# Performance work log

Measured on AMD Instinct MI355X. Metric: run time of the kernel, lower is better.

## Reference

```python
import jax, jax.numpy as jnp
import numpy as np

BEAM = 64  # beam_size from init (0 < 64 < num_tags=1024)


def setup_inputs() -> dict:
    key = jax.random.key(0)
    k1, k2, k3 = jax.random.split(key, 3)
    S, T = 16384, 1024  # seq_len, num_tags
    scores = jax.random.normal(k1, (S, T), dtype=jnp.float32)
    weights = jax.random.normal(k2, (T, T), dtype=jnp.float32) * 0.1  # CRF transition params
    tags = jax.random.randint(k3, (S,), 0, T)
    return {"scores": scores, "weights": weights, "tags": tags}


def reference(scores, weights, tags):
    # scores: [S, T] emission scores (output of base RNN tagger)
    # weights: [T, T] CRF transition scores, tags: [S] gold tags (eval mode, tags given)
    best_scores, best_tags = jax.lax.top_k(scores, BEAM)  # [S, B]

    def step(carry, x):
        vit, fwd = carry                     # each [B]
        prev_t, cur_t, cur_s = x             # [B], [B], [B]
        w = weights[prev_t[:, None], cur_t[None, :]]          # [B, B] transition lookup
        vals_v = vit[:, None] + cur_s[None, :] + w            # Viterbi lattice [B, B]
        vals_f = fwd[:, None] + cur_s[None, :] + w            # forward lattice [B, B]
        new_vit = vals_v.max(axis=0)
        bp = jnp.argmax(vals_v, axis=0)                       # backpointer [B]
        new_fwd = jax.nn.logsumexp(vals_f, axis=0)
        return (new_vit, new_fwd), bp

    init = (best_scores[0], best_scores[0])
    (vit, fwd), bps = jax.lax.scan(
        step, init, (best_tags[:-1], best_tags[1:], best_scores[1:]))  # bps: [S-1, B]

    # Viterbi backtrace
    last = jnp.argmax(vit)

    def back(idx, bp):
        new = bp[idx]
        return new, new

    _, idxs = jax.lax.scan(back, last, bps, reverse=True)     # indices for steps 0..S-2
    best_indices = jnp.concatenate([idxs, last[None]])        # [S]
    predicted_tags = jnp.take_along_axis(best_tags, best_indices[:, None], axis=1)[:, 0]

    # negative log-likelihood
    base = jnp.take_along_axis(scores, tags[:, None], axis=1).sum()
    crf = weights[tags[:-1], tags[1:]].sum()
    logZ = jax.nn.logsumexp(fwd)
    logprob = base + crf - logZ
    return predicted_tags, -logprob
```

## Files before the change

### kernel.cpp

```cpp
#include <hip/hip_runtime.h>
#include <math.h>

#define S 16384
#define T 1024
#define B 64
#define NSTEP (S - 1)
#define CH 64
#define NC 256
#define PD 8

#define K2E 1.44269504088896340736f
#define LN2 0.69314718055994530942f
#define LN64 4.15888308335967186f

static constexpr size_t SZ_SB   = (size_t)S * B * 4;
static constexpr size_t OFF_BS  = 0;
static constexpr size_t OFF_BT  = OFF_BS + SZ_SB;
static constexpr size_t OFF_VIT = OFF_BT + SZ_SB;
static constexpr size_t OFF_BP  = OFF_VIT + SZ_SB;
static constexpr size_t OFF_GT  = OFF_BP + SZ_SB;
static constexpr size_t SZ_GT   = (size_t)NC * B * B * 4;
static constexpr size_t OFF_MAP = OFF_GT + SZ_GT;
static constexpr size_t OFF_BND = OFF_MAP + (size_t)NC * B * 4;
static constexpr size_t OFF_SCAL= OFF_BND + 4096;
static constexpr size_t OFF_W   = OFF_SCAL + 4096;
static constexpr size_t SZ_W    = (size_t)NSTEP * B * B * 4;

__global__ __launch_bounds__(64) void k_topk(const float* __restrict__ scores,
                                             float* __restrict__ bs, int* __restrict__ bt) {
  int row = blockIdx.x;
  int lane = threadIdx.x;
  const float* rp = scores + (size_t)row * T;
  float v[16];
#pragma unroll
  for (int k = 0; k < 16; ++k) v[k] = rp[k * 64 + lane];
  for (int b = 0; b < B; ++b) {
    float lv = v[0]; int lk = 0;
#pragma unroll
    for (int k = 1; k < 16; ++k) {
      if (v[k] > lv) { lv = v[k]; lk = k; }
    }
    float bv = lv; int be = lk * 64 + lane;
#pragma unroll
    for (int off = 32; off >= 1; off >>= 1) {
      float ov = __shfl_xor(bv, off);
      int   oe = __shfl_xor(be, off);
      if (ov > bv || (ov == bv && oe < be)) { bv = ov; be = oe; }
    }
    if (lane == 0) {
      bs[(size_t)row * B + b] = bv;
      bt[(size_t)row * B + b] = be;
    }
    int bk = be >> 6, bl = be & 63;
#pragma unroll
    for (int k = 0; k < 16; ++k) {
      if (k == bk && lane == bl) v[k] = -3.0e38f;
    }
  }
}

__global__ __launch_bounds__(256) void k_pregather(const float* __restrict__ wt,
                                                   const int* __restrict__ bt,
                                                   float* __restrict__ Wp,
                                                   int tbase, int ns) {
  size_t n = (size_t)blockIdx.x * 256 + threadIdx.x;
  int i4  = (int)(n & 15);
  int j   = (int)((n >> 4) & 63);
  int rel = (int)(n >> 10);
  if (rel >= ns) return;
  int tm1 = tbase - 1 + rel;
  int ct = bt[(size_t)(tm1 + 1) * B + j];
  const int* pt = bt + (size_t)tm1 * B + i4 * 4;
  float4 o;
  o.x = wt[(size_t)pt[0] * T + ct];
  o.y = wt[(size_t)pt[1] * T + ct];
  o.z = wt[(size_t)pt[2] * T + ct];
  o.w = wt[(size_t)pt[3] * T + ct];
  ((float4*)Wp)[n] = o;
}

__global__ __launch_bounds__(512) void k_seqvit_seg(const float* __restrict__ bs,
                                                    const float* __restrict__ Wp,
                                                    float* __restrict__ vit,
                                                    int t0, int ns) {
  __shared__ alignas(16) float vb[2][B];
  int tid = threadIdx.x, w = tid >> 6, l = tid & 63;
  int j = (w << 3) | (l >> 3);
  int i0 = (l & 7) << 3;
  if (tid < B) {
    float v0 = (t0 == 1) ? bs[tid] : vit[(size_t)(t0 - 1) * B + tid];
    vb[0][tid] = v0;
    if (t0 == 1) vit[tid] = v0;
  }
  const float* wrow = Wp + (size_t)j * B + i0;
  float4 wa[PD], wc[PD];
  float ss[PD];
#pragma unroll
  for (int d = 0; d < PD; ++d) {
    if (d < ns) {
      const float4* q = (const float4*)(wrow + (size_t)d * B * B);
      wa[d] = q[0]; wc[d] = q[1];
      ss[d] = bs[(size_t)(t0 + d) * B + j];
    }
  }
  __syncthreads();
  int p = 0;
  for (int k0 = 0; k0 < ns; k0 += PD) {
#pragma unroll
    for (int ph = 0; ph < PD; ++ph) {
      int k = k0 + ph;
      if (k < ns) {
        float4 A = wa[ph], C = wc[ph];
        float s = ss[ph];
        const float4* vr = (const float4*)&vb[p][i0];
        float4 va = vr[0], v2 = vr[1];
        float m0 = fmaxf((va.x + s) + A.x, (va.y + s) + A.y);
        float m1 = fmaxf((va.z + s) + A.z, (va.w + s) + A.w);
        float m2 = fmaxf((v2.x + s) + C.x, (v2.y + s) + C.y);
        float m3 = fmaxf((v2.z + s) + C.z, (v2.w + s) + C.w);
        float m = fmaxf(fmaxf(m0, m1), fmaxf(m2, m3));
        m = fmaxf(m, __shfl_xor(m, 1));
        m = fmaxf(m, __shfl_xor(m, 2));
        m = fmaxf(m, __shfl_xor(m, 4));
        if (k + PD < ns) {
          const float4* q = (const float4*)(wrow + (size_t)(k + PD) * B * B);
          wa[ph] = q[0]; wc[ph] = q[1];
          ss[ph] = bs[(size_t)(t0 + k + PD) * B + j];
        }
        if ((l & 7) == 0) {
          vb[1 - p][j] = m;
          vit[(size_t)(t0 + k) * B + j] = m;
        }
        __syncthreads();
        p ^= 1;
      }
    }
  }
}

__global__ __launch_bounds__(512) void k_seqvit_slow(const float* __restrict__ bs,
                                                     const int* __restrict__ bt,
                                                     const float* __restrict__ wt,
                                                     float* __restrict__ vit) {
  __shared__ float vitbuf[B];
  __shared__ int tagbuf[B];
  __shared__ float part[2][8][B];
  int tid = threadIdx.x, w = tid >> 6, j = tid & 63;
  float v0 = bs[j];
  vitbuf[j] = v0;
  tagbuf[j] = bt[j];
  if (w == 0) vit[j] = v0;
  __syncthreads();
  for (int t = 1; t <= NSTEP; ++t) {
    float ss = bs[(size_t)t * B + j];
    int ct = bt[(size_t)t * B + j];
    float m = -3.0e38f;
#pragma unroll
    for (int e = 0; e < 8; ++e) {
      float vi = vitbuf[(w << 3) + e];
      int   pt = tagbuf[(w << 3) + e];
      float wv = wt[(size_t)pt * T + ct];
      m = fmaxf(m, (vi + ss) + wv);
    }
    int par = t & 1;
    part[par][w][j] = m;
    __syncthreads();
    float nv = part[par][0][j];
#pragma unroll
    for (int ww = 1; ww < 8; ++ww) nv = fmaxf(nv, part[par][ww][j]);
    vitbuf[j] = nv;
    tagbuf[j] = ct;
    if (w == 0) vit[(size_t)t * B + j] = nv;
  }
}

__global__ __launch_bounds__(256) void k_fwdchunk(const float* __restrict__ bs,
                                                  const int* __restrict__ bt,
                                                  const float* __restrict__ Wp,
                                                  const float* __restrict__ wt,
                                                  float* __restrict__ Gt, int usePre) {
  __shared__ alignas(16) float Pt[2][B][68];
  __shared__ float X[B][B];
  __shared__ alignas(16) float Rk[B];
  __shared__ float Qi[B];
  __shared__ float pmx[4][B];
  __shared__ int ptl[B];
  int tid = threadIdx.x, r = tid >> 6, j = tid & 63;
  int c = blockIdx.x;
  int t0 = c * CH + 1;
  int t1 = min(c * CH + CH, NSTEP);
#pragma unroll
  for (int e = 0; e < 16; ++e) {
    int i = 16 * r + e;
    Pt[0][j][i] = (i == j) ? 1.0f : 0.0f;
  }
  if (r == 0) { Rk[j] = 0.0f; Qi[j] = 0.0f; }
  __syncthreads();
  int pb = 0;
  for (int t = t0; t <= t1; ++t) {
    float ev[16];
    if (usePre) {
      const float4* q = (const float4*)(Wp + (((size_t)(t - 1) * B + j) * B + 16 * r));
      float4 q0 = q[0], q1 = q[1], q2 = q[2], q3 = q[3];
      ev[0] = q0.x; ev[1] = q0.y; ev[2] = q0.z; ev[3] = q0.w;
      ev[4] = q1.x; ev[5] = q1.y; ev[6] = q1.z; ev[7] = q1.w;
      ev[8] = q2.x; ev[9] = q2.y; ev[10] = q2.z; ev[11] = q2.w;
      ev[12] = q3.x; ev[13] = q3.y; ev[14] = q3.z; ev[15] = q3.w;
    } else {
      if (tid < B) ptl[tid] = bt[(size_t)(t - 1) * B + tid];
      __syncthreads();
      int ct = bt[(size_t)t * B + j];
#pragma unroll
      for (int e = 0; e < 16; ++e) ev[e] = wt[(size_t)ptl[16 * r + e] * T + ct];
    }
    {
      const float4* rq = (const float4*)&Rk[16 * r];
      float4 r0 = rq[0], r1 = rq[1], r2 = rq[2], r3 = rq[3];
      ev[0] += r0.x; ev[1] += r0.y; ev[2] += r0.z; ev[3] += r0.w;
      ev[4] += r1.x; ev[5] += r1.y; ev[6] += r1.z; ev[7] += r1.w;
      ev[8] += r2.x; ev[9] += r2.y; ev[10] += r2.z; ev[11] += r2.w;
      ev[12] += r3.x; ev[13] += r3.y; ev[14] += r3.z; ev[15] += r3.w;
    }
    float pm = ev[0];
#pragma unroll
    for (int e = 1; e < 16; ++e) pm = fmaxf(pm, ev[e]);
    pmx[r][j] = pm;
    __syncthreads();
    float Mw = fmaxf(fmaxf(pmx[0][j], pmx[1][j]), fmaxf(pmx[2][j], pmx[3][j]));
#pragma unroll
    for (int e = 0; e < 16; ++e)
      X[16 * r + e][j] = exp2f(K2E * (ev[e] - Mw) - 6.0f);
    __syncthreads();
    if (r == 0) Rk[j] = (bs[(size_t)t * B + j] + Mw) + LN64;
    float acc[16];
#pragma unroll
    for (int e = 0; e < 16; ++e) acc[e] = 0.0f;
    for (int k = 0; k < B; ++k) {
      float xk = X[k][j];
      const float4* pr = (const float4*)&Pt[pb][k][16 * r];
      float4 p0 = pr[0], p1 = pr[1], p2 = pr[2], p3 = pr[3];
      acc[0] = fmaf(p0.x, xk, acc[0]);   acc[1] = fmaf(p0.y, xk, acc[1]);
      acc[2] = fmaf(p0.z, xk, acc[2]);   acc[3] = fmaf(p0.w, xk, acc[3]);
      acc[4] = fmaf(p1.x, xk, acc[4]);   acc[5] = fmaf(p1.y, xk, acc[5]);
      acc[6] = fmaf(p1.z, xk, acc[6]);   acc[7] = fmaf(p1.w, xk, acc[7]);
      acc[8] = fmaf(p2.x, xk, acc[8]);   acc[9] = fmaf(p2.y, xk, acc[9]);
      acc[10] = fmaf(p2.z, xk, acc[10]); acc[11] = fmaf(p2.w, xk, acc[11]);
      acc[12] = fmaf(p3.x, xk, acc[12]); acc[13] = fmaf(p3.y, xk, acc[13]);
      acc[14] = fmaf(p3.z, xk, acc[14]); acc[15] = fmaf(p3.w, xk, acc[15]);
    }
#pragma unroll
    for (int e = 0; e < 4; ++e) {
      float4 o;
      o.x = acc[4 * e]; o.y = acc[4 * e + 1]; o.z = acc[4 * e + 2]; o.w = acc[4 * e + 3];
      *(float4*)&Pt[1 - pb][j][16 * r + 4 * e] = o;
    }
    pb ^= 1;
    __syncthreads();
    if (((t - t0) & 15) == 15 && t != t1) {
      int i = j;
      float qm = Pt[pb][16 * r][i];
#pragma unroll
      for (int e = 1; e < 16; ++e) qm = fmaxf(qm, Pt[pb][16 * r + e][i]);
      pmx[r][i] = qm;
      __syncthreads();
      float qv = fmaxf(fmaxf(pmx[0][i], pmx[1][i]), fmaxf(pmx[2][i], pmx[3][i]));
      float inv = 1.0f / qv;
#pragma unroll
      for (int e = 0; e < 16; ++e) Pt[pb][16 * r + e][i] *= inv;
      if (r == 0) Qi[i] += LN2 * log2f(qv);
      __syncthreads();
    }
  }
  float rj = Rk[j];
#pragma unroll
  for (int e = 0; e < 16; ++e) {
    int i = 16 * r + e;
    float p = Pt[pb][j][i];
    float g = (p > 0.0f) ? (Qi[i] + rj + LN2 * log2f(p)) : -3.0e38f;
    Gt[((size_t)c * B + j) * B + i] = g;
  }
}

__global__ __launch_bounds__(256) void k_combine(const float* __restrict__ bs,
                                                 const float* __restrict__ Gt,
                                                 const float* __restrict__ scal,
                                                 float* __restrict__ out) {
  __shared__ alignas(16) float fbuf[B];
  __shared__ float pmm[2][4][B];
  __shared__ float pss[2][4][B];
  int tid = threadIdx.x, r = tid >> 6, j = tid & 63;
  fbuf[j] = bs[j];
  __syncthreads();
  for (int c = 0; c < NC; ++c) {
    const float4* gq = (const float4*)(Gt + ((size_t)c * B + j) * B + 16 * r);
    float4 g0 = gq[0], g1 = gq[1], g2 = gq[2], g3 = gq[3];
    const float4* fp = (const float4*)&fbuf[16 * r];
    float4 f0 = fp[0], f1 = fp[1], f2 = fp[2], f3 = fp[3];
    float a[16];
    a[0] = f0.x + g0.x; a[1] = f0.y + g0.y; a[2] = f0.z + g0.z; a[3] = f0.w + g0.w;
    a[4] = f1.x + g1.x; a[5] = f1.y + g1.y; a[6] = f1.z + g1.z; a[7] = f1.w + g1.w;
    a[8] = f2.x + g2.x; a[9] = f2.y + g2.y; a[10] = f2.z + g2.z; a[11] = f2.w + g2.w;
    a[12] = f3.x + g3.x; a[13] = f3.y + g3.y; a[14] = f3.z + g3.z; a[15] = f3.w + g3.w;
    float M = a[0];
#pragma unroll
    for (int u = 1; u < 16; ++u) M = fmaxf(M, a[u]);
    int pc = c & 1;
    pmm[pc][r][j] = M;
    __syncthreads();
    M = fmaxf(fmaxf(pmm[pc][0][j], pmm[pc][1][j]), fmaxf(pmm[pc][2][j], pmm[pc][3][j]));
    float ssum = 0.0f;
#pragma unroll
    for (int u = 0; u < 16; ++u) ssum += exp2f(K2E * (a[u] - M));
    pss[pc][r][j] = ssum;
    __syncthreads();
    float tot = pss[pc][0][j] + pss[pc][1][j] + pss[pc][2][j] + pss[pc][3][j];
    fbuf[j] = M + LN2 * log2f(tot);
  }
  __syncthreads();
  if (tid < 64) {
    float f = fbuf[tid];
    float M = f;
#pragma unroll
    for (int off = 32; off >= 1; off >>= 1) M = fmaxf(M, __shfl_xor(M, off));
    float sv = exp2f(K2E * (f - M));
#pragma unroll
    for (int off = 32; off >= 1; off >>= 1) sv += __shfl_xor(sv, off);
    if (tid == 0) out[S] = (M + LN2 * log2f(sv)) - scal[0];
  }
}

__global__ __launch_bounds__(256) void k_bp(const float* __restrict__ bs,
                                            const int* __restrict__ bt,
                                            const float* __restrict__ Wp,
                                            const float* __restrict__ wt,
                                            const float* __restrict__ vit,
                                            int* __restrict__ bp, int usePre) {
  int t = blockIdx.x + 1;
  int tid = threadIdx.x, r = tid >> 6, j = tid & 63;
  __shared__ alignas(16) float vl[B];
  __shared__ int ptl[B];
  __shared__ float pmv[4][B];
  __shared__ int pma[4][B];
  if (tid < B) {
    vl[tid] = vit[(size_t)(t - 1) * B + tid];
    ptl[tid] = usePre ? 0 : bt[(size_t)(t - 1) * B + tid];
  }
  __syncthreads();
  float s = bs[(size_t)t * B + j];
  float m; int a;
  if (usePre) {
    const float4* q = (const float4*)(Wp + (((size_t)(t - 1) * B + j) * B + 16 * r));
    float4 q0 = q[0], q1 = q[1], q2 = q[2], q3 = q[3];
    float wv[16] = {q0.x, q0.y, q0.z, q0.w, q1.x, q1.y, q1.z, q1.w,
                    q2.x, q2.y, q2.z, q2.w, q3.x, q3.y, q3.z, q3.w};
    m = (vl[16 * r] + s) + wv[0];
    a = 16 * r;
#pragma unroll
    for (int e = 1; e < 16; ++e) {
      float cv = (vl[16 * r + e] + s) + wv[e];
      if (cv > m) { m = cv; a = 16 * r + e; }
    }
  } else {
    int ct = bt[(size_t)t * B + j];
    m = -3.0e38f; a = 16 * r;
#pragma unroll
    for (int e = 0; e < 16; ++e) {
      float cv = (vl[16 * r + e] + s) + wt[(size_t)ptl[16 * r + e] * T + ct];
      if (cv > m) { m = cv; a = 16 * r + e; }
    }
  }
  pmv[r][j] = m; pma[r][j] = a;
  __syncthreads();
  if (r == 0) {
#pragma unroll
    for (int ww = 1; ww < 4; ++ww) {
      float om = pmv[ww][j];
      if (om > m) { m = om; a = pma[ww][j]; }
    }
    bp[(size_t)t * B + j] = a;
  }
}

__global__ __launch_bounds__(64) void k_chunkback(const int* __restrict__ bp,
                                                  int* __restrict__ map) {
  int c = blockIdx.x, lane = threadIdx.x;
  int t0 = c * CH + 1;
  int t1 = min(c * CH + CH, NSTEP);
  int nst = t1 - t0 + 1;
  __shared__ int bpl[CH][B];
  for (int tt = 0; tt < nst; ++tt) bpl[tt][lane] = bp[(size_t)(t0 + tt) * B + lane];
  __syncthreads();
  int cur = lane;
  for (int tt = nst - 1; tt >= 0; --tt) cur = bpl[tt][cur];
  map[c * B + lane] = cur;
}

__global__ __launch_bounds__(256) void k_bound(const float* __restrict__ vit,
                                               const int* __restrict__ map,
                                               int* __restrict__ bnd) {
  __shared__ unsigned char ml[NC * B];
  __shared__ int lastSh;
  int tid = threadIdx.x;
  for (int k = tid; k < NC * B; k += 256) ml[k] = (unsigned char)map[k];
  if (tid < 64) {
    float v = vit[(size_t)NSTEP * B + tid];
    int a = tid;
#pragma unroll
    for (int off = 32; off >= 1; off >>= 1) {
      float ov = __shfl_xor(v, off);
      int   oa = __shfl_xor(a, off);
      if (ov > v || (ov == v && oa < a)) { v = ov; a = oa; }
    }
    if (tid == 0) lastSh = a;
  }
  __syncthreads();
  if (tid == 0) {
    int cur = lastSh;
    bnd[NC] = cur;
    for (int c = NC - 1; c >= 0; --c) {
      cur = (int)ml[c * B + cur];
      bnd[c] = cur;
    }
  }
}

__global__ __launch_bounds__(64) void k_emit(const int* __restrict__ bp,
                                             const int* __restrict__ bnd,
                                             const int* __restrict__ bt,
                                             float* __restrict__ out) {
  int c = blockIdx.x, lane = threadIdx.x;
  int t0 = c * CH + 1;
  int t1 = min(c * CH + CH, NSTEP);
  int nst = t1 - t0 + 1;
  __shared__ int bpl[CH][B];
  __shared__ int idxl[CH];
  for (int tt = 0; tt < nst; ++tt) bpl[tt][lane] = bp[(size_t)(t0 + tt) * B + lane];
  __syncthreads();
  if (lane == 0) {
    int cur = bnd[c + 1];
    for (int p = t1 - 1; p >= t0 - 1; --p) {
      cur = bpl[p - (t0 - 1)][cur];
      idxl[p - (t0 - 1)] = cur;
    }
  }
  __syncthreads();
  int p = (t0 - 1) + lane;
  if (lane < nst) {
    int idx = idxl[lane];
    out[p] = (float)bt[(size_t)p * B + idx];
  }
  if (c == NC - 1 && lane == 0) {
    int last = bnd[NC];
    out[S - 1] = (float)bt[(size_t)(S - 1) * B + last];
  }
}

__global__ __launch_bounds__(256) void k_basecrf(const float* __restrict__ scores,
                                                 const float* __restrict__ wt,
                                                 const int* __restrict__ tg,
                                                 float* __restrict__ scal) {
  int n = blockIdx.x * 256 + threadIdx.x;
  float v = 0.0f;
  if (n < S) {
    v = scores[(size_t)n * T + tg[n]];
  } else if (n < S + S - 1) {
    int m = n - S;
    v = wt[(size_t)tg[m] * T + tg[m + 1]];
  }
#pragma unroll
  for (int off = 32; off >= 1; off >>= 1) v += __shfl_xor(v, off);
  if ((threadIdx.x & 63) == 0) atomicAdd(scal, v);
}

extern "C" void kernel_launch(void* const* d_in, const int* in_sizes, int n_in,
                              void* d_out, int out_size, void* d_ws, size_t ws_size,
                              hipStream_t stream) {
  const float* scores  = (const float*)d_in[0];
  const float* weights = (const float*)d_in[1];
  const int*   tags    = (const int*)d_in[2];
  float* out = (float*)d_out;
  char* ws = (char*)d_ws;

  if (ws_size < OFF_W) return;

  float* bs   = (float*)(ws + OFF_BS);
  int*   bt   = (int*)(ws + OFF_BT);
  float* vit  = (float*)(ws + OFF_VIT);
  int*   bp   = (int*)(ws + OFF_BP);
  float* Gt   = (float*)(ws + OFF_GT);
  int*   map  = (int*)(ws + OFF_MAP);
  int*   bnd  = (int*)(ws + OFF_BND);
  float* scal = (float*)(ws + OFF_SCAL);
  float* Wp   = (float*)(ws + OFF_W);

  size_t avail = ws_size - OFF_W;
  long seg = (long)(avail / ((size_t)B * B * 4));
  if (seg > NSTEP) seg = NSTEP;
  int useSeg = (seg >= 512) ? 1 : 0;
  int usePre = (seg >= NSTEP) ? 1 : 0;

  hipMemsetAsync(ws + OFF_SCAL, 0, 64, stream);

  k_topk<<<S, 64, 0, stream>>>(scores, bs, bt);
  k_basecrf<<<(2 * S - 1 + 255) / 256, 256, 0, stream>>>(scores, weights, tags, scal);

  if (useSeg) {
    for (int t0 = 1; t0 <= NSTEP; t0 += (int)seg) {
      int ns = (int)((NSTEP - t0 + 1 < seg) ? (NSTEP - t0 + 1) : seg);
      int nblk = (int)(((size_t)ns * 1024 + 255) / 256);
      k_pregather<<<nblk, 256, 0, stream>>>(weights, bt, Wp, t0, ns);
      k_seqvit_seg<<<1, 512, 0, stream>>>(bs, Wp, vit, t0, ns);
    }
  } else {
    k_seqvit_slow<<<1, 512, 0, stream>>>(bs, bt, weights, vit);
  }

  k_fwdchunk<<<NC, 256, 0, stream>>>(bs, bt, Wp, weights, Gt, usePre);
  k_bp<<<NSTEP, 256, 0, stream>>>(bs, bt, Wp, weights, vit, bp, usePre);
  k_combine<<<1, 256, 0, stream>>>(bs, Gt, scal, out);
  k_chunkback<<<NC, 64, 0, stream>>>(bp, map);
  k_bound<<<1, 256, 0, stream>>>(vit, map, bnd);
  k_emit<<<NC, 64, 0, stream>>>(bp, bnd, bt, out);
}
```

Measured before the change: 7.879 ms.

## Replace per-step barrier in sequential Viterbi with LDS flag handshakes across four waves

After: 14.90 ms. +89.1%, slower.

```diff
diff --git a/kernel.cpp b/kernel.cpp
--- a/kernel.cpp
+++ b/kernel.cpp
@@ -7,7 +7,7 @@
 #define NSTEP (S - 1)
 #define CH 64
 #define NC 256
-#define PD 8
+#define VPD 6
 
 #define K2E 1.44269504088896340736f
 #define LN2 0.69314718055994530942f
@@ -25,6 +25,13 @@
 static constexpr size_t OFF_SCAL= OFF_BND + 4096;
 static constexpr size_t OFF_W   = OFF_SCAL + 4096;
 static constexpr size_t SZ_W    = (size_t)NSTEP * B * B * 4;
+
+__device__ __forceinline__ void pin4(float4& a) {
+  asm volatile("" : "+v"(a.x), "+v"(a.y), "+v"(a.z), "+v"(a.w));
+}
+__device__ __forceinline__ void pin1(float& a) {
+  asm volatile("" : "+v"(a));
+}
 
 __global__ __launch_bounds__(64) void k_topk(const float* __restrict__ scores,
                                              float* __restrict__ bs, int* __restrict__ bt) {
@@ -79,60 +86,76 @@
   ((float4*)Wp)[n] = o;
 }
 
-__global__ __launch_bounds__(512) void k_seqvit_seg(const float* __restrict__ bs,
-                                                    const float* __restrict__ Wp,
-                                                    float* __restrict__ vit,
-                                                    int t0, int ns) {
+__global__ __launch_bounds__(256, 1) void k_seqvit_flag(const float* __restrict__ bs,
+                                                        const float* __restrict__ Wp,
+                                                        float* __restrict__ vit,
+                                                        int t0, int ns) {
   __shared__ alignas(16) float vb[2][B];
+  __shared__ unsigned int flags[4];
   int tid = threadIdx.x, w = tid >> 6, l = tid & 63;
-  int j = (w << 3) | (l >> 3);
-  int i0 = (l & 7) << 3;
+  int q = l >> 2, r = l & 3;
+  int j = (w << 4) | q;
+  int i0 = r << 4;
   if (tid < B) {
     float v0 = (t0 == 1) ? bs[tid] : vit[(size_t)(t0 - 1) * B + tid];
     vb[0][tid] = v0;
     if (t0 == 1) vit[tid] = v0;
   }
+  if (l == 0) flags[w] = 0u;
   const float* wrow = Wp + (size_t)j * B + i0;
-  float4 wa[PD], wc[PD];
-  float ss[PD];
-#pragma unroll
-  for (int d = 0; d < PD; ++d) {
+  float4 wr[VPD][4];
+  float ss[VPD];
+#pragma unroll
+  for (int d = 0; d < VPD; ++d) {
     if (d < ns) {
-      const float4* q = (const float4*)(wrow + (size_t)d * B * B);
-      wa[d] = q[0]; wc[d] = q[1];
+      const float4* qp = (const float4*)(wrow + (size_t)d * B * B);
+      wr[d][0] = qp[0]; wr[d][1] = qp[1]; wr[d][2] = qp[2]; wr[d][3] = qp[3];
       ss[d] = bs[(size_t)(t0 + d) * B + j];
-    }
-  }
-  __syncthreads();
-  int p = 0;
-  for (int k0 = 0; k0 < ns; k0 += PD) {
-#pragma unroll
-    for (int ph = 0; ph < PD; ++ph) {
+      pin4(wr[d][0]); pin4(wr[d][1]); pin4(wr[d][2]); pin4(wr[d][3]);
+      pin1(ss[d]);
+    }
+  }
+  __syncthreads();
+  for (int k0 = 0; k0 < ns; k0 += VPD) {
+#pragma unroll
+    for (int ph = 0; ph < VPD; ++ph) {
       int k = k0 + ph;
       if (k < ns) {
-        float4 A = wa[ph], C = wc[ph];
+        unsigned int want = (unsigned int)k;
+        while (__hip_atomic_load(&flags[r], __ATOMIC_ACQUIRE,
+                                 __HIP_MEMORY_SCOPE_WORKGROUP) < want) {}
+        int p = k & 1;
+        const float4* vr = (const float4*)&vb[p][i0];
+        float4 v0 = vr[0], v1 = vr[1], v2 = vr[2], v3 = vr[3];
         float s = ss[ph];
-        const float4* vr = (const float4*)&vb[p][i0];
-        float4 va = vr[0], v2 = vr[1];
-        float m0 = fmaxf((va.x + s) + A.x, (va.y + s) + A.y);
-        float m1 = fmaxf((va.z + s) + A.z, (va.w + s) + A.w);
-        float m2 = fmaxf((v2.x + s) + C.x, (v2.y + s) + C.y);
-        float m3 = fmaxf((v2.z + s) + C.z, (v2.w + s) + C.w);
+        float4 A = wr[ph][0], Bq = wr[ph][1], Cq = wr[ph][2], Dq = wr[ph][3];
+        float m0 = fmaxf(fmaxf((v0.x + s) + A.x,  (v0.y + s) + A.y),
+                         fmaxf((v0.z + s) + A.z,  (v0.w + s) + A.w));
+        float m1 = fmaxf(fmaxf((v1.x + s) + Bq.x, (v1.y + s) + Bq.y),
+                         fmaxf((v1.z + s) + Bq.z, (v1.w + s) + Bq.w));
+        float m2 = fmaxf(fmaxf((v2.x + s) + Cq.x, (v2.y + s) + Cq.y),
+                         fmaxf((v2.z + s) + Cq.z, (v2.w + s) + Cq.w));
+        float m3 = fmaxf(fmaxf((v3.x + s) + Dq.x, (v3.y + s) + Dq.y),
+                         fmaxf((v3.z + s) + Dq.z, (v3.w + s) + Dq.w));
         float m = fmaxf(fmaxf(m0, m1), fmaxf(m2, m3));
-        m = fmaxf(m, __shfl_xor(m, 1));
-        m = fmaxf(m, __shfl_xor(m, 2));
-        m = fmaxf(m, __shfl_xor(m, 4));
-        if (k + PD < ns) {
-          const float4* q = (const float4*)(wrow + (size_t)(k + PD) * B * B);
-          wa[ph] = q[0]; wc[ph] = q[1];
-          ss[ph] = bs[(size_t)(t0 + k + PD) * B + j];
+        m = fmaxf(m, __int_as_float(__builtin_amdgcn_mov_dpp(
+                        __float_as_int(m), 0xB1, 0xF, 0xF, true)));
+        m = fmaxf(m, __int_as_float(__builtin_amdgcn_mov_dpp(
+                        __float_as_int(m), 0x4E, 0xF, 0xF, true)));
+        if (k + VPD < ns) {
+          const float4* qp = (const float4*)(wrow + (size_t)(k + VPD) * B * B);
+          wr[ph][0] = qp[0]; wr[ph][1] = qp[1]; wr[ph][2] = qp[2]; wr[ph][3] = qp[3];
+          ss[ph] = bs[(size_t)(t0 + k + VPD) * B + j];
+          pin4(wr[ph][0]); pin4(wr[ph][1]); pin4(wr[ph][2]); pin4(wr[ph][3]);
+          pin1(ss[ph]);
         }
-        if ((l & 7) == 0) {
+        if (r == 0) {
           vb[1 - p][j] = m;
           vit[(size_t)(t0 + k) * B + j] = m;
         }
-        __syncthreads();
-        p ^= 1;
+        if (l == 0)
+          __hip_atomic_store(&flags[w], (unsigned int)(k + 1), __ATOMIC_RELEASE,
+                             __HIP_MEMORY_SCOPE_WORKGROUP);
       }
     }
   }
@@ -509,7 +532,7 @@
       int ns = (int)((NSTEP - t0 + 1 < seg) ? (NSTEP - t0 + 1) : seg);
       int nblk = (int)(((size_t)ns * 1024 + 255) / 256);
       k_pregather<<<nblk, 256, 0, stream>>>(weights, bt, Wp, t0, ns);
-      k_seqvit_seg<<<1, 512, 0, stream>>>(bs, Wp, vit, t0, ns);
+      k_seqvit_flag<<<1, 256, 0, stream>>>(bs, Wp, vit, t0, ns);
     }
   } else {
     k_seqvit_slow<<<1, 512, 0, stream>>>(bs, bt, weights, vit);
```

## Stream sequential Viterbi transition tiles through LDS with async global-to-LDS loads

Applied to the files above, without the earlier changes.

Result: slower. 11.30 ms (+43.4%).

```diff
diff --git a/kernel.cpp b/kernel.cpp
--- a/kernel.cpp
+++ b/kernel.cpp
@@ -7,7 +7,7 @@
 #define NSTEP (S - 1)
 #define CH 64
 #define NC 256
-#define PD 8
+#define DW 2
 
 #define K2E 1.44269504088896340736f
 #define LN2 0.69314718055994530942f
@@ -25,6 +25,19 @@
 static constexpr size_t OFF_SCAL= OFF_BND + 4096;
 static constexpr size_t OFF_W   = OFF_SCAL + 4096;
 static constexpr size_t SZ_W    = (size_t)NSTEP * B * B * 4;
+
+__device__ __forceinline__ void glds16(const float* g, float* lds) {
+  __builtin_amdgcn_global_load_lds((const __attribute__((address_space(1))) void*)g,
+                                   (__attribute__((address_space(3))) void*)lds, 16, 0, 0);
+}
+__device__ __forceinline__ void glds4(const float* g, float* lds) {
+  __builtin_amdgcn_global_load_lds((const __attribute__((address_space(1))) void*)g,
+                                   (__attribute__((address_space(3))) void*)lds, 4, 0, 0);
+}
+__device__ __forceinline__ void dummy_vm(const float* g) {
+  float t;
+  asm volatile("global_load_dword %0, %1, off" : "=v"(t) : "v"(g));
+}
 
 __global__ __launch_bounds__(64) void k_topk(const float* __restrict__ scores,
                                              float* __restrict__ bs, int* __restrict__ bt) {
@@ -79,62 +92,88 @@
   ((float4*)Wp)[n] = o;
 }
 
-__global__ __launch_bounds__(512) void k_seqvit_seg(const float* __restrict__ bs,
+#define SEQSTEP(KK, Wr, Sr, Wpre, Spre)                                        \
+  {                                                                            \
+    int k_ = (KK);                                                             \
+    if (k_ < ns) {                                                             \
+      int kp_ = k_ + DW; if (kp_ >= ns) kp_ = ns - 1;                          \
+      const float* gp_ = gw + (size_t)kp_ * 4096;                              \
+      glds16(gp_,       Wpre);       glds16(gp_ + 256, (Wpre) + 256);          \
+      glds16(gp_ + 512, (Wpre) + 512); glds16(gp_ + 768, (Wpre) + 768);        \
+      glds4(gs + (size_t)kp_ * 64, Spre);                                      \
+      asm volatile("s_waitcnt vmcnt(12) lgkmcnt(0)\n\ts_barrier" ::: "memory"); \
+      float s_ = (Sr)[j];                                                      \
+      const float4* wv_ = (const float4*)((Wr) + (jp << 6) + i0);              \
+      float4 wa_ = wv_[0], wb_ = wv_[1], wc_ = wv_[2], wd_ = wv_[3];           \
+      const float4* vv_ = (const float4*)&vbuf[p][i0];                         \
+      float4 va_ = vv_[0], v2_ = vv_[1], v3_ = vv_[2], v4_ = vv_[3];           \
+      float m_ =            (va_.x + s_) + wa_.x;                              \
+      m_ = fmaxf(m_, (va_.y + s_) + wa_.y);                                    \
+      m_ = fmaxf(m_, (va_.z + s_) + wa_.z);                                    \
+      m_ = fmaxf(m_, (va_.w + s_) + wa_.w);                                    \
+      m_ = fmaxf(m_, (v2_.x + s_) + wb_.x);                                    \
+      m_ = fmaxf(m_, (v2_.y + s_) + wb_.y);                                    \
+      m_ = fmaxf(m_, (v2_.z + s_) + wb_.z);                                    \
+      m_ = fmaxf(m_, (v2_.w + s_) + wb_.w);                                    \
+      m_ = fmaxf(m_, (v3_.x + s_) + wc_.x);                                    \
+      m_ = fmaxf(m_, (v3_.y + s_) + wc_.y);                                    \
+      m_ = fmaxf(m_, (v3_.z + s_) + wc_.z);                                    \
+      m_ = fmaxf(m_, (v3_.w + s_) + wc_.w);                                    \
+      m_ = fmaxf(m_, (v4_.x + s_) + wd_.x);                                    \
+      m_ = fmaxf(m_, (v4_.y + s_) + wd_.y);                                    \
+      m_ = fmaxf(m_, (v4_.z + s_) + wd_.z);                                    \
+      m_ = fmaxf(m_, (v4_.w + s_) + wd_.w);                                    \
+      m_ = fmaxf(m_, __shfl_xor(m_, 1));                                       \
+      m_ = fmaxf(m_, __shfl_xor(m_, 2));                                       \
+      if ((l & 3) == 0) {                                                      \
+        vbuf[1 - p][j] = m_;                                                   \
+        vit[(size_t)(t0 + k_) * B + j] = m_;                                   \
+      }                                                                        \
+      p ^= 1;                                                                  \
+    }                                                                          \
+  }
+
+__global__ __launch_bounds__(256) void k_seqvit_lds(const float* __restrict__ bs,
                                                     const float* __restrict__ Wp,
                                                     float* __restrict__ vit,
                                                     int t0, int ns) {
-  __shared__ alignas(16) float vb[2][B];
+  __shared__ float Wa[4][1024];
+  __shared__ float Wb[4][1024];
+  __shared__ float Wc[4][1024];
+  __shared__ float Sa[4][64];
+  __shared__ float Sb[4][64];
+  __shared__ float Sc[4][64];
+  __shared__ alignas(16) float vbuf[2][B];
   int tid = threadIdx.x, w = tid >> 6, l = tid & 63;
-  int j = (w << 3) | (l >> 3);
-  int i0 = (l & 7) << 3;
+  int jp = l >> 2;
+  int j  = (w << 4) | jp;
+  int i0 = (l & 3) << 4;
   if (tid < B) {
     float v0 = (t0 == 1) ? bs[tid] : vit[(size_t)(t0 - 1) * B + tid];
-    vb[0][tid] = v0;
+    vbuf[0][tid] = v0;
     if (t0 == 1) vit[tid] = v0;
   }
-  const float* wrow = Wp + (size_t)j * B + i0;
-  float4 wa[PD], wc[PD];
-  float ss[PD];
-#pragma unroll
-  for (int d = 0; d < PD; ++d) {
-    if (d < ns) {
-      const float4* q = (const float4*)(wrow + (size_t)d * B * B);
-      wa[d] = q[0]; wc[d] = q[1];
-      ss[d] = bs[(size_t)(t0 + d) * B + j];
-    }
-  }
-  __syncthreads();
+  __syncthreads();
+  const float* gw = Wp + (size_t)w * 1024 + (size_t)l * 4;
+  const float* gs = bs + (size_t)t0 * B + l;
+  float* wA = &Wa[w][0]; float* wB = &Wb[w][0]; float* wC = &Wc[w][0];
+  float* sA = &Sa[w][0]; float* sB = &Sb[w][0]; float* sC = &Sc[w][0];
+
+  {
+    glds16(gw, wA); glds16(gw + 256, wA + 256); glds16(gw + 512, wA + 512); glds16(gw + 768, wA + 768);
+    glds4(gs, sA);
+    dummy_vm(bs);
+    int k1 = (1 < ns) ? 1 : 0;
+    const float* g1 = gw + (size_t)k1 * 4096;
+    glds16(g1, wB); glds16(g1 + 256, wB + 256); glds16(g1 + 512, wB + 512); glds16(g1 + 768, wB + 768);
+    glds4(gs + (size_t)k1 * 64, sB);
+    dummy_vm(bs);
+  }
   int p = 0;
-  for (int k0 = 0; k0 < ns; k0 += PD) {
-#pragma unroll
-    for (int ph = 0; ph < PD; ++ph) {
-      int k = k0 + ph;
-      if (k < ns) {
-        float4 A = wa[ph], C = wc[ph];
-        float s = ss[ph];
-        const float4* vr = (const float4*)&vb[p][i0];
-        float4 va = vr[0], v2 = vr[1];
-        float m0 = fmaxf((va.x + s) + A.x, (va.y + s) + A.y);
-        float m1 = fmaxf((va.z + s) + A.z, (va.w + s) + A.w);
-        float m2 = fmaxf((v2.x + s) + C.x, (v2.y + s) + C.y);
-        float m3 = fmaxf((v2.z + s) + C.z, (v2.w + s) + C.w);
-        float m = fmaxf(fmaxf(m0, m1), fmaxf(m2, m3));
-        m = fmaxf(m, __shfl_xor(m, 1));
-        m = fmaxf(m, __shfl_xor(m, 2));
-        m = fmaxf(m, __shfl_xor(m, 4));
-        if (k + PD < ns) {
-          const float4* q = (const float4*)(wrow + (size_t)(k + PD) * B * B);
-          wa[ph] = q[0]; wc[ph] = q[1];
-          ss[ph] = bs[(size_t)(t0 + k + PD) * B + j];
-        }
-        if ((l & 7) == 0) {
-          vb[1 - p][j] = m;
-          vit[(size_t)(t0 + k) * B + j] = m;
-        }
-        __syncthreads();
-        p ^= 1;
-      }
-    }
+  for (int k0 = 0; k0 < ns; k0 += 3) {
+    SEQSTEP(k0 + 0, wA, sA, wC, sC);
+    SEQSTEP(k0 + 1, wB, sB, wA, sA);
+    SEQSTEP(k0 + 2, wC, sC, wB, sB);
   }
 }
 
@@ -509,7 +548,7 @@
       int ns = (int)((NSTEP - t0 + 1 < seg) ? (NSTEP - t0 + 1) : seg);
       int nblk = (int)(((size_t)ns * 1024 + 255) / 256);
       k_pregather<<<nblk, 256, 0, stream>>>(weights, bt, Wp, t0, ns);
-      k_seqvit_seg<<<1, 512, 0, stream>>>(bs, Wp, vit, t0, ns);
+      k_seqvit_lds<<<1, 256, 0, stream>>>(bs, Wp, vit, t0, ns);
     }
   } else {
     k_seqvit_slow<<<1, 512, 0, stream>>>(bs, bt, weights, vit);
```

## Parallelize Viterbi recurrence via chunked max-plus transfer matrices

Applied to the files above, without the earlier changes.

After: 27.16 ms. 245% more time.

```diff
diff --git a/kernel.cpp b/kernel.cpp
--- a/kernel.cpp
+++ b/kernel.cpp
@@ -7,11 +7,11 @@
 #define NSTEP (S - 1)
 #define CH 64
 #define NC 256
-#define PD 8
 
 #define K2E 1.44269504088896340736f
 #define LN2 0.69314718055994530942f
 #define LN64 4.15888308335967186f
+#define NEGBIG -3.0e38f
 
 static constexpr size_t SZ_SB   = (size_t)S * B * 4;
 static constexpr size_t OFF_BS  = 0;
@@ -23,7 +23,8 @@
 static constexpr size_t OFF_MAP = OFF_GT + SZ_GT;
 static constexpr size_t OFF_BND = OFF_MAP + (size_t)NC * B * 4;
 static constexpr size_t OFF_SCAL= OFF_BND + 4096;
-static constexpr size_t OFF_W   = OFF_SCAL + 4096;
+static constexpr size_t OFF_VBND= OFF_SCAL + 4096;
+static constexpr size_t OFF_W   = OFF_VBND + 66560;
 static constexpr size_t SZ_W    = (size_t)NSTEP * B * B * 4;
 
 __global__ __launch_bounds__(64) void k_topk(const float* __restrict__ scores,
@@ -79,62 +80,153 @@
   ((float4*)Wp)[n] = o;
 }
 
-__global__ __launch_bounds__(512) void k_seqvit_seg(const float* __restrict__ bs,
-                                                    const float* __restrict__ Wp,
-                                                    float* __restrict__ vit,
-                                                    int t0, int ns) {
-  __shared__ alignas(16) float vb[2][B];
-  int tid = threadIdx.x, w = tid >> 6, l = tid & 63;
-  int j = (w << 3) | (l >> 3);
-  int i0 = (l & 7) << 3;
+__global__ __launch_bounds__(256) void k_vitchunk(const float* __restrict__ bs,
+                                                  const float* __restrict__ Wp,
+                                                  float* __restrict__ Pv) {
+  __shared__ alignas(16) float Pt[2][B][68];
+  __shared__ float X[B][B];
+  int tid = threadIdx.x, r = tid >> 6, j = tid & 63;
+  int c = blockIdx.x;
+  int t0 = c * CH + 1;
+  int t1 = min(c * CH + CH, NSTEP);
+#pragma unroll
+  for (int e = 0; e < 16; ++e) {
+    int i = 16 * r + e;
+    Pt[0][j][i] = (i == j) ? 0.0f : NEGBIG;
+  }
+  __syncthreads();
+  int pb = 0;
+  for (int t = t0; t <= t1; ++t) {
+    const float4* q = (const float4*)(Wp + (((size_t)(t - 1) * B + j) * B + 16 * r));
+    float4 q0 = q[0], q1 = q[1], q2 = q[2], q3 = q[3];
+    float sj = bs[(size_t)t * B + j];
+    X[16 * r + 0][j]  = sj + q0.x;  X[16 * r + 1][j]  = sj + q0.y;
+    X[16 * r + 2][j]  = sj + q0.z;  X[16 * r + 3][j]  = sj + q0.w;
+    X[16 * r + 4][j]  = sj + q1.x;  X[16 * r + 5][j]  = sj + q1.y;
+    X[16 * r + 6][j]  = sj + q1.z;  X[16 * r + 7][j]  = sj + q1.w;
+    X[16 * r + 8][j]  = sj + q2.x;  X[16 * r + 9][j]  = sj + q2.y;
+    X[16 * r + 10][j] = sj + q2.z;  X[16 * r + 11][j] = sj + q2.w;
+    X[16 * r + 12][j] = sj + q3.x;  X[16 * r + 13][j] = sj + q3.y;
+    X[16 * r + 14][j] = sj + q3.z;  X[16 * r + 15][j] = sj + q3.w;
+    __syncthreads();
+    float acc[16];
+#pragma unroll
+    for (int e = 0; e < 16; ++e) acc[e] = NEGBIG;
+    for (int k = 0; k < B; ++k) {
+      float xk = X[k][j];
+      const float4* pr = (const float4*)&Pt[pb][k][16 * r];
+      float4 p0 = pr[0], p1 = pr[1], p2 = pr[2], p3 = pr[3];
+      acc[0]  = fmaxf(acc[0],  p0.x + xk); acc[1]  = fmaxf(acc[1],  p0.y + xk);
+      acc[2]  = fmaxf(acc[2],  p0.z + xk); acc[3]  = fmaxf(acc[3],  p0.w + xk);
+      acc[4]  = fmaxf(acc[4],  p1.x + xk); acc[5]  = fmaxf(acc[5],  p1.y + xk);
+      acc[6]  = fmaxf(acc[6],  p1.z + xk); acc[7]  = fmaxf(acc[7],  p1.w + xk);
+      acc[8]  = fmaxf(acc[8],  p2.x + xk); acc[9]  = fmaxf(acc[9],  p2.y + xk);
+      acc[10] = fmaxf(acc[10], p2.z + xk); acc[11] = fmaxf(acc[11], p2.w + xk);
+      acc[12] = fmaxf(acc[12], p3.x + xk); acc[13] = fmaxf(acc[13], p3.y + xk);
+      acc[14] = fmaxf(acc[14], p3.z + xk); acc[15] = fmaxf(acc[15], p3.w + xk);
+    }
+#pragma unroll
+    for (int e = 0; e < 4; ++e) {
+      float4 o;
+      o.x = acc[4 * e]; o.y = acc[4 * e + 1]; o.z = acc[4 * e + 2]; o.w = acc[4 * e + 3];
+      *(float4*)&Pt[1 - pb][j][16 * r + 4 * e] = o;
+    }
+    pb ^= 1;
+    __syncthreads();
+  }
+#pragma unroll
+  for (int e = 0; e < 4; ++e) {
+    float4 o;
+    o.x = Pt[pb][j][16 * r + 4 * e + 0];
+    o.y = Pt[pb][j][16 * r + 4 * e + 1];
+    o.z = Pt[pb][j][16 * r + 4 * e + 2];
+    o.w = Pt[pb][j][16 * r + 4 * e + 3];
+    *(float4*)(Pv + ((size_t)c * B + j) * B + 16 * r + 4 * e) = o;
+  }
+}
+
+__global__ __launch_bounds__(512) void k_vitcombine(const float* __restrict__ bs,
+                                                    const float* __restrict__ Pv,
+                                                    float* __restrict__ vbnd) {
+  __shared__ alignas(16) float vc[2][B];
+  int tid = threadIdx.x;
+  int j = tid >> 3, q = tid & 7, i0 = q << 3;
   if (tid < B) {
-    float v0 = (t0 == 1) ? bs[tid] : vit[(size_t)(t0 - 1) * B + tid];
-    vb[0][tid] = v0;
-    if (t0 == 1) vit[tid] = v0;
-  }
-  const float* wrow = Wp + (size_t)j * B + i0;
-  float4 wa[PD], wc[PD];
-  float ss[PD];
-#pragma unroll
-  for (int d = 0; d < PD; ++d) {
-    if (d < ns) {
-      const float4* q = (const float4*)(wrow + (size_t)d * B * B);
-      wa[d] = q[0]; wc[d] = q[1];
-      ss[d] = bs[(size_t)(t0 + d) * B + j];
-    }
+    float v = bs[tid];
+    vc[0][tid] = v;
+    vbnd[tid] = v;
   }
   __syncthreads();
   int p = 0;
-  for (int k0 = 0; k0 < ns; k0 += PD) {
-#pragma unroll
-    for (int ph = 0; ph < PD; ++ph) {
-      int k = k0 + ph;
-      if (k < ns) {
-        float4 A = wa[ph], C = wc[ph];
-        float s = ss[ph];
-        const float4* vr = (const float4*)&vb[p][i0];
-        float4 va = vr[0], v2 = vr[1];
-        float m0 = fmaxf((va.x + s) + A.x, (va.y + s) + A.y);
-        float m1 = fmaxf((va.z + s) + A.z, (va.w + s) + A.w);
-        float m2 = fmaxf((v2.x + s) + C.x, (v2.y + s) + C.y);
-        float m3 = fmaxf((v2.z + s) + C.z, (v2.w + s) + C.w);
-        float m = fmaxf(fmaxf(m0, m1), fmaxf(m2, m3));
-        m = fmaxf(m, __shfl_xor(m, 1));
-        m = fmaxf(m, __shfl_xor(m, 2));
-        m = fmaxf(m, __shfl_xor(m, 4));
-        if (k + PD < ns) {
-          const float4* q = (const float4*)(wrow + (size_t)(k + PD) * B * B);
-          wa[ph] = q[0]; wc[ph] = q[1];
-          ss[ph] = bs[(size_t)(t0 + k + PD) * B + j];
-        }
-        if ((l & 7) == 0) {
-          vb[1 - p][j] = m;
-          vit[(size_t)(t0 + k) * B + j] = m;
-        }
-        __syncthreads();
-        p ^= 1;
+  for (int c = 0; c < NC; ++c) {
+    const float4* gp = (const float4*)(Pv + ((size_t)c * B + j) * B + i0);
+    float4 p0 = gp[0], p1 = gp[1];
+    const float4* vv = (const float4*)&vc[p][i0];
+    float4 v0 = vv[0], v1 = vv[1];
+    float m =          v0.x + p0.x;
+    m = fmaxf(m, v0.y + p0.y);
+    m = fmaxf(m, v0.z + p0.z);
+    m = fmaxf(m, v0.w + p0.w);
+    m = fmaxf(m, v1.x + p1.x);
+    m = fmaxf(m, v1.y + p1.y);
+    m = fmaxf(m, v1.z + p1.z);
+    m = fmaxf(m, v1.w + p1.w);
+    m = fmaxf(m, __shfl_xor(m, 1));
+    m = fmaxf(m, __shfl_xor(m, 2));
+    m = fmaxf(m, __shfl_xor(m, 4));
+    if (q == 0) {
+      vc[1 - p][j] = m;
+      vbnd[(size_t)(c + 1) * B + j] = m;
+    }
+    __syncthreads();
+    p ^= 1;
+  }
+}
+
+__global__ __launch_bounds__(256) void k_vitsteps(const float* __restrict__ bs,
+                                                  const float* __restrict__ Wp,
+                                                  const float* __restrict__ vbnd,
+                                                  int* __restrict__ bp) {
+  __shared__ alignas(16) float vc[2][B];
+  __shared__ float pmv[4][B];
+  __shared__ int pma[4][B];
+  int tid = threadIdx.x, r = tid >> 6, j = tid & 63;
+  int c = blockIdx.x;
+  int t0 = c * CH + 1;
+  int t1 = min(c * CH + CH, NSTEP);
+  if (tid < B) vc[0][tid] = vbnd[(size_t)c * B + tid];
+  __syncthreads();
+  int p = 0;
+  for (int t = t0; t <= t1; ++t) {
+    const float4* q4 = (const float4*)(Wp + (((size_t)(t - 1) * B + j) * B + 16 * r));
+    float4 w0 = q4[0], w1 = q4[1], w2 = q4[2], w3 = q4[3];
+    float s = bs[(size_t)t * B + j];
+    const float4* vv = (const float4*)&vc[p][16 * r];
+    float4 a = vv[0], b = vv[1], cc = vv[2], d = vv[3];
+    float wv[16] = {w0.x, w0.y, w0.z, w0.w, w1.x, w1.y, w1.z, w1.w,
+                    w2.x, w2.y, w2.z, w2.w, w3.x, w3.y, w3.z, w3.w};
+    float vl[16] = {a.x, a.y, a.z, a.w, b.x, b.y, b.z, b.w,
+                    cc.x, cc.y, cc.z, cc.w, d.x, d.y, d.z, d.w};
+    float m = (vl[0] + s) + wv[0];
+    int aidx = 16 * r;
+#pragma unroll
+    for (int e = 1; e < 16; ++e) {
+      float cv = (vl[e] + s) + wv[e];
+      if (cv > m) { m = cv; aidx = 16 * r + e; }
+    }
+    pmv[r][j] = m; pma[r][j] = aidx;
+    __syncthreads();
+    if (r == 0) {
+#pragma unroll
+      for (int ww = 1; ww < 4; ++ww) {
+        float om = pmv[ww][j];
+        if (om > m) { m = om; aidx = pma[ww][j]; }
       }
-    }
+      bp[(size_t)t * B + j] = aidx;
+      vc[1 - p][j] = m;
+    }
+    __syncthreads();
+    p ^= 1;
   }
 }
 
@@ -154,13 +246,13 @@
   for (int t = 1; t <= NSTEP; ++t) {
     float ss = bs[(size_t)t * B + j];
     int ct = bt[(size_t)t * B + j];
-    float m = -3.0e38f;
+    float m = NEGBIG;
 #pragma unroll
     for (int e = 0; e < 8; ++e) {
       float vi = vitbuf[(w << 3) + e];
       int   pt = tagbuf[(w << 3) + e];
-      float wv = wt[(size_t)pt * T + ct];
-      m = fmaxf(m, (vi + ss) + wv);
+      float wvv = wt[(size_t)pt * T + ct];
+      m = fmaxf(m, (vi + ss) + wvv);
     }
     int par = t & 1;
     part[par][w][j] = m;
@@ -276,7 +368,7 @@
   for (int e = 0; e < 16; ++e) {
     int i = 16 * r + e;
     float p = Pt[pb][j][i];
-    float g = (p > 0.0f) ? (Qi[i] + rj + LN2 * log2f(p)) : -3.0e38f;
+    float g = (p > 0.0f) ? (Qi[i] + rj + LN2 * log2f(p)) : NEGBIG;
     Gt[((size_t)c * B + j) * B + i] = g;
   }
 }
@@ -331,10 +423,9 @@
 
 __global__ __launch_bounds__(256) void k_bp(const float* __restrict__ bs,
                                             const int* __restrict__ bt,
-                                            const float* __restrict__ Wp,
                                             const float* __restrict__ wt,
                                             const float* __restrict__ vit,
-                                            int* __restrict__ bp, int usePre) {
+                                            int* __restrict__ bp) {
   int t = blockIdx.x + 1;
   int tid = threadIdx.x, r = tid >> 6, j = tid & 63;
   __shared__ alignas(16) float vl[B];
@@ -343,31 +434,16 @@
   __shared__ int pma[4][B];
   if (tid < B) {
     vl[tid] = vit[(size_t)(t - 1) * B + tid];
-    ptl[tid] = usePre ? 0 : bt[(size_t)(t - 1) * B + tid];
+    ptl[tid] = bt[(size_t)(t - 1) * B + tid];
   }
   __syncthreads();
   float s = bs[(size_t)t * B + j];
-  float m; int a;
-  if (usePre) {
-    const float4* q = (const float4*)(Wp + (((size_t)(t - 1) * B + j) * B + 16 * r));
-    float4 q0 = q[0], q1 = q[1], q2 = q[2], q3 = q[3];
-    float wv[16] = {q0.x, q0.y, q0.z, q0.w, q1.x, q1.y, q1.z, q1.w,
-                    q2.x, q2.y, q2.z, q2.w, q3.x, q3.y, q3.z, q3.w};
-    m = (vl[16 * r] + s) + wv[0];
-    a = 16 * r;
-#pragma unroll
-    for (int e = 1; e < 16; ++e) {
-      float cv = (vl[16 * r + e] + s) + wv[e];
-      if (cv > m) { m = cv; a = 16 * r + e; }
-    }
-  } else {
-    int ct = bt[(size_t)t * B + j];
-    m = -3.0e38f; a = 16 * r;
-#pragma unroll
-    for (int e = 0; e < 16; ++e) {
-      float cv = (vl[16 * r + e] + s) + wt[(size_t)ptl[16 * r + e] * T + ct];
-      if (cv > m) { m = cv; a = 16 * r + e; }
-    }
+  int ct = bt[(size_t)t * B + j];
+  float m = NEGBIG; int a = 16 * r;
+#pragma unroll
+  for (int e = 0; e < 16; ++e) {
+    float cv = (vl[16 * r + e] + s) + wt[(size_t)ptl[16 * r + e] * T + ct];
+    if (cv > m) { m = cv; a = 16 * r + e; }
   }
   pmv[r][j] = m; pma[r][j] = a;
   __syncthreads();
@@ -395,7 +471,7 @@
   map[c * B + lane] = cur;
 }
 
-__global__ __launch_bounds__(256) void k_bound(const float* __restrict__ vit,
+__global__ __launch_bounds__(256) void k_bound(const float* __restrict__ vfin,
                                                const int* __restrict__ map,
                                                int* __restrict__ bnd) {
   __shared__ unsigned char ml[NC * B];
@@ -403,7 +479,7 @@
   int tid = threadIdx.x;
   for (int k = tid; k < NC * B; k += 256) ml[k] = (unsigned char)map[k];
   if (tid < 64) {
-    float v = vit[(size_t)NSTEP * B + tid];
+    float v = vfin[tid];
     int a = tid;
 #pragma unroll
     for (int off = 32; off >= 1; off >>= 1) {
@@ -486,39 +562,41 @@
   float* bs   = (float*)(ws + OFF_BS);
   int*   bt   = (int*)(ws + OFF_BT);
   float* vit  = (float*)(ws + OFF_VIT);
+  float* Pv   = (float*)(ws + OFF_VIT);
   int*   bp   = (int*)(ws + OFF_BP);
   float* Gt   = (float*)(ws + OFF_GT);
   int*   map  = (int*)(ws + OFF_MAP);
   int*   bnd  = (int*)(ws + OFF_BND);
   float* scal = (float*)(ws + OFF_SCAL);
+  float* vbnd = (float*)(ws + OFF_VBND);
   float* Wp   = (float*)(ws + OFF_W);
 
   size_t avail = ws_size - OFF_W;
-  long seg = (long)(avail / ((size_t)B * B * 4));
-  if (seg > NSTEP) seg = NSTEP;
-  int useSeg = (seg >= 512) ? 1 : 0;
-  int usePre = (seg >= NSTEP) ? 1 : 0;
+  int full = (avail >= SZ_W) ? 1 : 0;
 
   hipMemsetAsync(ws + OFF_SCAL, 0, 64, stream);
 
   k_topk<<<S, 64, 0, stream>>>(scores, bs, bt);
   k_basecrf<<<(2 * S - 1 + 255) / 256, 256, 0, stream>>>(scores, weights, tags, scal);
 
-  if (useSeg) {
-    for (int t0 = 1; t0 <= NSTEP; t0 += (int)seg) {
-      int ns = (int)((NSTEP - t0 + 1 < seg) ? (NSTEP - t0 + 1) : seg);
-      int nblk = (int)(((size_t)ns * 1024 + 255) / 256);
-      k_pregather<<<nblk, 256, 0, stream>>>(weights, bt, Wp, t0, ns);
-      k_seqvit_seg<<<1, 512, 0, stream>>>(bs, Wp, vit, t0, ns);
-    }
+  if (full) {
+    int nblk = (int)(((size_t)NSTEP * 1024 + 255) / 256);
+    k_pregather<<<nblk, 256, 0, stream>>>(weights, bt, Wp, 1, NSTEP);
+    k_vitchunk<<<NC, 256, 0, stream>>>(bs, Wp, Pv);
+    k_vitcombine<<<1, 512, 0, stream>>>(bs, Pv, vbnd);
+    k_vitsteps<<<NC, 256, 0, stream>>>(bs, Wp, vbnd, bp);
+    k_fwdchunk<<<NC, 256, 0, stream>>>(bs, bt, Wp, weights, Gt, 1);
+    k_combine<<<1, 256, 0, stream>>>(bs, Gt, scal, out);
+    k_chunkback<<<NC, 64, 0, stream>>>(bp, map);
+    k_bound<<<1, 256, 0, stream>>>(vbnd + (size_t)NC * B, map, bnd);
+    k_emit<<<NC, 64, 0, stream>>>(bp, bnd, bt, out);
   } else {
     k_seqvit_slow<<<1, 512, 0, stream>>>(bs, bt, weights, vit);
-  }
-
-  k_fwdchunk<<<NC, 256, 0, stream>>>(bs, bt, Wp, weights, Gt, usePre);
-  k_bp<<<NSTEP, 256, 0, stream>>>(bs, bt, Wp, weights, vit, bp, usePre);
-  k_combine<<<1, 256, 0, stream>>>(bs, Gt, scal, out);
-  k_chunkback<<<NC, 64, 0, stream>>>(bp, map);
-  k_bound<<<1, 256, 0, stream>>>(vit, map, bnd);
-  k_emit<<<NC, 64, 0, stream>>>(bp, bnd, bt, out);
-}
+    k_fwdchunk<<<NC, 256, 0, stream>>>(bs, bt, Wp, weights, Gt, 0);
+    k_bp<<<NSTEP, 256, 0, stream>>>(bs, bt, weights, vit, bp);
+    k_combine<<<1, 256, 0, stream>>>(bs, Gt, scal, out);
+    k_chunkback<<<NC, 64, 0, stream>>>(bp, map);
+    k_bound<<<1, 256, 0, stream>>>(vit + (size_t)NSTEP * B, map, bnd);
+    k_emit<<<NC, 64, 0, stream>>>(bp, bnd, bt, out);
+  }
+}
```
